# Kernel tuning notes

Hardware: AMD Instinct MI355X
Metric: run time of the kernel (lower is better)

## Reference

```python
import jax, jax.numpy as jnp
import numpy as np

INPUT_DIM, HIDDEN_DIM, OUTPUT_DIM = 64, 256, 64
# AutoNCP(256, 64): inter_and_command=192, command=int(0.4*192)=76, inter=116, motor=64
INTER, COMMAND, MOTOR = 116, 76, 64
SENSORY_FANOUT, INTER_FANOUT, MOTOR_FANIN = 58, 38, 38
B, T = 512, 256


def setup_inputs() -> dict:
    rng = np.random.default_rng(0)
    key = jax.random.key(0)
    d = {}
    # NCP wiring sparsity (binary masks; ncps takes abs() so polarity is irrelevant for the mask)
    m0 = np.zeros((INTER, INPUT_DIM), np.float32)
    for i in range(INPUT_DIM):
        m0[rng.choice(INTER, SENSORY_FANOUT, replace=False), i] = 1.0
    m1 = np.zeros((COMMAND, INTER), np.float32)
    for i in range(INTER):
        m1[rng.choice(COMMAND, INTER_FANOUT, replace=False), i] = 1.0
    m2 = np.zeros((MOTOR, COMMAND), np.float32)
    for o in range(MOTOR):
        m2[o, rng.choice(COMMAND, MOTOR_FANIN, replace=False)] = 1.0
    dims = [(INPUT_DIM, INTER, m0), (INTER, COMMAND, m1), (COMMAND, MOTOR, m2)]
    for l, (fi, h, m) in enumerate(dims):
        cat = fi + h
        # mask shape [h, fi+h]: sparse prev-layer block + all-ones recurrent block (as in WiredCfCCell)
        d[f"mask_{l}"] = jnp.asarray(np.concatenate([m, np.ones((h, h), np.float32)], axis=1))
        bound = float(1.0 / np.sqrt(cat))
        for nm in ("ff1", "ff2", "ta", "tb"):
            key, k1, k2 = jax.random.split(key, 3)
            d[f"w_{nm}_{l}"] = jax.random.uniform(k1, (h, cat), minval=-bound, maxval=bound, dtype=jnp.float32)
            d[f"b_{nm}_{l}"] = jax.random.uniform(k2, (h,), minval=-bound, maxval=bound, dtype=jnp.float32)
    key, k1, k2, kx = jax.random.split(key, 4)
    bound = float(1.0 / np.sqrt(OUTPUT_DIM))
    d["w_fc"] = jax.random.uniform(k1, (OUTPUT_DIM, OUTPUT_DIM), minval=-bound, maxval=bound, dtype=jnp.float32)
    d["b_fc"] = jax.random.uniform(k2, (OUTPUT_DIM,), minval=-bound, maxval=bound, dtype=jnp.float32)
    d["x"] = jax.random.normal(kx, (B, T, INPUT_DIM), dtype=jnp.float32)
    return d


def _cfc_cell(xin, h, w1, b1, w2, b2, wa, ba, wb, bb, mask):
    # CfCCell 'default' mode, no backbone, ts = 1.0
    cat = jnp.concatenate([xin, h], axis=-1)          # [B, fi+h]
    ff1 = jnp.tanh(cat @ (w1 * mask).T + b1)
    ff2 = jnp.tanh(cat @ (w2 * mask).T + b2)
    t_interp = jax.nn.sigmoid(cat @ wa.T + ba + cat @ wb.T + bb)  # sigmoid(t_a*1.0 + t_b)
    return ff1 * (1.0 - t_interp) + t_interp * ff2


def _forward(x, layer_params, masks, w_fc, b_fc):
    bsz = x.shape[0]
    h0 = tuple(jnp.zeros((bsz, h), x.dtype) for h in (INTER, COMMAND, MOTOR))

    def step(hs, xt):
        inp = xt
        new = []
        for l in range(3):  # inter -> command -> motor (structurally distinct layers)
            h = _cfc_cell(inp, hs[l], *layer_params[l], masks[l])
            inp = h
            new.append(h)
        return tuple(new), inp  # motor-layer output per step

    _, ys = jax.lax.scan(step, h0, jnp.swapaxes(x, 0, 1))
    y = jnp.swapaxes(ys, 0, 1)  # [B, T, MOTOR]
    return y @ w_fc.T + b_fc


def reference(x, w_ff1_0, b_ff1_0, w_ff2_0, b_ff2_0, w_ta_0, b_ta_0, w_tb_0, b_tb_0,
              w_ff1_1, b_ff1_1, w_ff2_1, b_ff2_1, w_ta_1, b_ta_1, w_tb_1, b_tb_1,
              w_ff1_2, b_ff1_2, w_ff2_2, b_ff2_2, w_ta_2, b_ta_2, w_tb_2, b_tb_2,
              w_fc, b_fc, mask_0, mask_1, mask_2):
    layer_params = [
        (w_ff1_0, b_ff1_0, w_ff2_0, b_ff2_0, w_ta_0, b_ta_0, w_tb_0, b_tb_0),
        (w_ff1_1, b_ff1_1, w_ff2_1, b_ff2_1, w_ta_1, b_ta_1, w_tb_1, b_tb_1),
        (w_ff1_2, b_ff1_2, w_ff2_2, b_ff2_2, w_ta_2, b_ta_2, w_tb_2, b_tb_2),
    ]
    return _forward(x, layer_params, (mask_0, mask_1, mask_2), w_fc, b_fc)
```

## Files before the change

kernel.cpp:

```cpp
#include <hip/hip_runtime.h>

typedef _Float16 f16x8 __attribute__((ext_vector_type(8)));
typedef _Float16 f16x4 __attribute__((ext_vector_type(4)));
typedef float f32x4 __attribute__((ext_vector_type(4)));

#define NTH 512
#define SEQT 256
#define LD0 200
#define LD1 200
#define LD2 168

struct KArgs { const float* in[30]; float* out; };

__device__ __forceinline__ float fast_tanh(float x) {
  return __fdividef(2.0f, 1.0f + __expf(-2.0f * x)) - 1.0f;
}
__device__ __forceinline__ float fast_sig(float x) {
  return __fdividef(1.0f, 1.0f + __expf(-x));
}

__device__ __forceinline__ f32x4 mfma16(f16x8 a, f16x8 b, f32x4 c) {
  return __builtin_amdgcn_mfma_f32_16x16x32_f16(a, b, c, 0, 0, 0);
}

__device__ __forceinline__ f16x4 combine3(const f32x4 acc[3]) {
  f16x4 v;
  #pragma unroll
  for (int q = 0; q < 4; ++q) {
    const float ff1 = fast_tanh(acc[0][q]);
    const float ff2 = fast_tanh(acc[1][q]);
    const float ti  = fast_sig(acc[2][q]);
    v[q] = (_Float16)(ff1 + ti * (ff2 - ff1));
  }
  return v;
}

template<int BASE, int KT>
__device__ __forceinline__ void load_tile(f16x8* wW, const float* W1, const float* W2,
                                          const float* Wa, const float* Wb,
                                          const float* Mk, int n, int CAT, int H, int kb) {
  #pragma unroll
  for (int kt = 0; kt < KT; ++kt) {
    #pragma unroll
    for (int m = 0; m < 3; ++m) {
      f16x8 f;
      #pragma unroll
      for (int j = 0; j < 8; ++j) {
        const int k = kt * 32 + kb + j;
        float v = 0.f;
        if (n < H && k < CAT) {
          if (m == 0)      v = W1[n*CAT+k] * Mk[n*CAT+k];
          else if (m == 1) v = W2[n*CAT+k] * Mk[n*CAT+k];
          else             v = Wa[n*CAT+k] + Wb[n*CAT+k];
        }
        f[j] = (_Float16)v;
      }
      wW[BASE + m*KT + kt] = f;
    }
  }
}

template<int KT>
__device__ __forceinline__ void loadB(f16x8* B, const _Float16* c, int LD, int r, int kb) {
  #pragma unroll
  for (int kt = 0; kt < KT; ++kt)
    B[kt] = *reinterpret_cast<const f16x8*>(c + r*LD + kt*32 + kb);
}

template<int BASE, int KT>
__device__ __forceinline__ void mma_tile(f32x4 acc[3], const f16x8* wW, const f16x8* B) {
  #pragma unroll
  for (int kt = 0; kt < KT; ++kt)
    #pragma unroll
    for (int m = 0; m < 3; ++m)
      acc[m] = mfma16(wW[BASE + m*KT + kt], B[kt], acc[m]);
}

__device__ __forceinline__ void init3(f32x4 acc[3], const float* sb, int bs, int n0) {
  #pragma unroll
  for (int m = 0; m < 3; ++m)
    acc[m] = *reinterpret_cast<const f32x4*>(sb + m*bs + n0);
}

__device__ __forceinline__ f16x8 loadB8u(const _Float16* p) {
  const f16x4 a = *reinterpret_cast<const f16x4*>(p);
  const f16x4 b = *reinterpret_cast<const f16x4*>(p + 4);
  f16x8 v;
  v[0]=a[0]; v[1]=a[1]; v[2]=a[2]; v[3]=a[3];
  v[4]=b[0]; v[5]=b[1]; v[6]=b[2]; v[7]=b[3];
  return v;
}

__global__ __launch_bounds__(NTH, 2) void ncp_fused(KArgs args) {
  __shared__ __align__(16) _Float16 c0[2][16 * LD0];
  __shared__ __align__(16) _Float16 c1[2][16 * LD1];
  __shared__ __align__(16) _Float16 c2[2][16 * LD2];
  __shared__ __align__(16) _Float16 wt3[15 * 64 * 8];
  __shared__ float b0s[3 * 128], b1s[3 * 80], b2s[3 * 64];

  const int tid  = threadIdx.x;
  const int w    = tid >> 6;
  const int lane = tid & 63;
  const int r    = lane & 15;
  const int g    = lane >> 4;
  const int kb   = g * 8;
  const int wgBase = blockIdx.x * 16;
  const float* __restrict__ xg = args.in[29];
  float* __restrict__ out = args.out;

  f16x8 wW[36], wfc[2];
  f32x4 bfc = {0.f, 0.f, 0.f, 0.f};
  if (w < 4) {
    load_tile<0, 6>(wW, args.in[1], args.in[3], args.in[5], args.in[7], args.in[0],
                    (2*w)*16 + r, 180, 116, kb);
    load_tile<18, 6>(wW, args.in[1], args.in[3], args.in[5], args.in[7], args.in[0],
                     (2*w+1)*16 + r, 180, 116, kb);
    #pragma unroll
    for (int kt = 0; kt < 2; ++kt) {
      f16x8 f;
      #pragma unroll
      for (int j = 0; j < 8; ++j)
        f[j] = (_Float16)args.in[27][(w*16 + r)*64 + kt*32 + kb + j];
      wfc[kt] = f;
    }
    #pragma unroll
    for (int q = 0; q < 4; ++q) bfc[q] = args.in[28][w*16 + 4*g + q];
  } else if (w < 6) {
    load_tile<0, 6>(wW, args.in[10], args.in[12], args.in[14], args.in[16], args.in[9],
                    (2*(w-4))*16 + r, 192, 76, kb);
    load_tile<18, 6>(wW, args.in[10], args.in[12], args.in[14], args.in[16], args.in[9],
                     (2*(w-4)+1)*16 + r, 192, 76, kb);
  } else if (w == 6) {
    load_tile<0, 6>(wW, args.in[10], args.in[12], args.in[14], args.in[16], args.in[9],
                    64 + r, 192, 76, kb);
    load_tile<18, 5>(wW, args.in[19], args.in[21], args.in[23], args.in[25], args.in[18],
                     r, 140, 64, kb);
  } else {
    load_tile<0, 5>(wW, args.in[19], args.in[21], args.in[23], args.in[25], args.in[18],
                    16 + r, 140, 64, kb);
    load_tile<15, 5>(wW, args.in[19], args.in[21], args.in[23], args.in[25], args.in[18],
                     32 + r, 140, 64, kb);
  }

  for (int u = tid; u < 15 * 64; u += NTH) {
    const int ln = u & 63;
    const int ff = u >> 6;
    const int kt = ff % 5, m = ff / 5;
    const int n  = 48 + (ln & 15);
    const int kbb = (ln >> 4) * 8;
    f16x8 f;
    #pragma unroll
    for (int j = 0; j < 8; ++j) {
      const int k = kt*32 + kbb + j;
      float v = 0.f;
      if (k < 140) {
        if (m == 0)      v = args.in[19][n*140+k] * args.in[18][n*140+k];
        else if (m == 1) v = args.in[21][n*140+k] * args.in[18][n*140+k];
        else             v = args.in[23][n*140+k] + args.in[25][n*140+k];
      }
      f[j] = (_Float16)v;
    }
    *reinterpret_cast<f16x8*>(wt3 + (size_t)u * 8) = f;
  }
  if (tid < 128) {
    b0s[tid]       = (tid < 116) ? args.in[2][tid] : 0.f;
    b0s[128 + tid] = (tid < 116) ? args.in[4][tid] : 0.f;
    b0s[256 + tid] = (tid < 116) ? args.in[6][tid] + args.in[8][tid] : 0.f;
  }
  if (tid < 80) {
    b1s[tid]      = (tid < 76) ? args.in[11][tid] : 0.f;
    b1s[80 + tid] = (tid < 76) ? args.in[13][tid] : 0.f;
    b1s[160 + tid]= (tid < 76) ? args.in[15][tid] + args.in[17][tid] : 0.f;
  }
  if (tid < 64) {
    b2s[tid]       = args.in[20][tid];
    b2s[64 + tid]  = args.in[22][tid];
    b2s[128 + tid] = args.in[24][tid] + args.in[26][tid];
  }
  for (int i = tid; i < 2 * 16 * LD0; i += NTH) c0[0][i] = (_Float16)0.f;
  for (int i = tid; i < 2 * 16 * LD1; i += NTH) c1[0][i] = (_Float16)0.f;
  for (int i = tid; i < 2 * 16 * LD2; i += NTH) c2[0][i] = (_Float16)0.f;
  __syncthreads();
  {
    const int rr = tid >> 6, cc = tid & 63;
    c0[0][rr * LD0 + cc]       = (_Float16)xg[((size_t)(wgBase + rr) * SEQT + 0) * 64 + cc];
    c0[0][(8 + rr) * LD0 + cc] = (_Float16)xg[((size_t)(wgBase + 8 + rr) * SEQT + 0) * 64 + cc];
  }
  __syncthreads();

  #pragma unroll 1
  for (int p = 0; p < SEQT + 3; ++p) {
    const int cur = p & 1, nxt = cur ^ 1;

    float xr0, xr1;
    {
      const int tn = (p + 1 < SEQT) ? p + 1 : SEQT - 1;
      xr0 = xg[((size_t)(wgBase + (tid >> 6)) * SEQT + tn) * 64 + (tid & 63)];
      xr1 = xg[((size_t)(wgBase + 8 + (tid >> 6)) * SEQT + tn) * 64 + (tid & 63)];
    }

    if (w < 4) {
      if (p >= 3) {
        f32x4 acc = bfc;
        #pragma unroll
        for (int kt = 0; kt < 2; ++kt) {
          const f16x8 b = loadB8u(c2[cur] + r * LD2 + 76 + kt * 32 + kb);
          acc = mfma16(wfc[kt], b, acc);
        }
        *reinterpret_cast<f32x4*>(out + ((size_t)(wgBase + r) * SEQT + (p - 3)) * 64 + w * 16 + 4 * g) = acc;
      }
      if (p < SEQT) {
        f16x8 B[6]; loadB<6>(B, c0[cur], LD0, r, kb);
        f32x4 aA[3], aB[3];
        const int nA = (2 * w) * 16 + 4 * g;
        const int nB = (2 * w + 1) * 16 + 4 * g;
        init3(aA, b0s, 128, nA);
        init3(aB, b0s, 128, nB);
        mma_tile<0, 6>(aA, wW, B);
        mma_tile<18, 6>(aB, wW, B);
        const f16x4 vA = combine3(aA);
        const f16x4 vB = combine3(aB);
        *reinterpret_cast<f16x4*>(c1[nxt] + r * LD1 + nA)      = vA;
        *reinterpret_cast<f16x4*>(c0[nxt] + r * LD0 + 64 + nA) = vA;
        if (nB < 116) {
          *reinterpret_cast<f16x4*>(c1[nxt] + r * LD1 + nB)      = vB;
          *reinterpret_cast<f16x4*>(c0[nxt] + r * LD0 + 64 + nB) = vB;
        }
      }
    } else if (w < 6) {
      if (p >= 1 && p < SEQT + 1) {
        f16x8 B[6]; loadB<6>(B, c1[cur], LD1, r, kb);
        f32x4 aA[3], aB[3];
        const int nA = (2 * (w - 4)) * 16 + 4 * g;
        const int nB = (2 * (w - 4) + 1) * 16 + 4 * g;
        init3(aA, b1s, 80, nA);
        init3(aB, b1s, 80, nB);
        mma_tile<0, 6>(aA, wW, B);
        mma_tile<18, 6>(aB, wW, B);
        const f16x4 vA = combine3(aA);
        const f16x4 vB = combine3(aB);
        *reinterpret_cast<f16x4*>(c1[nxt] + r * LD1 + 116 + nA) = vA;
        *reinterpret_cast<f16x4*>(c2[nxt] + r * LD2 + nA)       = vA;
        *reinterpret_cast<f16x4*>(c1[nxt] + r * LD1 + 116 + nB) = vB;
        *reinterpret_cast<f16x4*>(c2[nxt] + r * LD2 + nB)       = vB;
      }
    } else if (w == 6) {
      if (p >= 1 && p < SEQT + 1) {
        f16x8 B[6]; loadB<6>(B, c1[cur], LD1, r, kb);
        f32x4 a4[3];
        const int n4 = 64 + 4 * g;
        init3(a4, b1s, 80, n4);
        mma_tile<0, 6>(a4, wW, B);
        const f16x4 v4 = combine3(a4);
        if (n4 < 76) {
          *reinterpret_cast<f16x4*>(c1[nxt] + r * LD1 + 116 + n4) = v4;
          *reinterpret_cast<f16x4*>(c2[nxt] + r * LD2 + n4)       = v4;
        }
      }
      if (p >= 2 && p < SEQT + 2) {
        f16x8 B[5]; loadB<5>(B, c2[cur], LD2, r, kb);
        f32x4 a0[3];
        const int nn = 4 * g;
        init3(a0, b2s, 64, nn);
        mma_tile<18, 5>(a0, wW, B);
        const f16x4 v0 = combine3(a0);
        *reinterpret_cast<f16x4*>(c2[nxt] + r * LD2 + 76 + nn) = v0;
      }
    } else {
      if (p >= 2 && p < SEQT + 2) {
        f16x8 B[5]; loadB<5>(B, c2[cur], LD2, r, kb);
        f32x4 a1[3], a2[3], a3[3];
        const int n1 = 16 + 4 * g, n2 = 32 + 4 * g, n3 = 48 + 4 * g;
        init3(a1, b2s, 64, n1);
        init3(a2, b2s, 64, n2);
        init3(a3, b2s, 64, n3);
        mma_tile<0, 5>(a1, wW, B);
        mma_tile<15, 5>(a2, wW, B);
        #pragma unroll
        for (int kt = 0; kt < 5; ++kt) {
          #pragma unroll
          for (int m = 0; m < 3; ++m) {
            const f16x8 a = *reinterpret_cast<const f16x8*>(wt3 + (size_t)((m * 5 + kt) * 64 + lane) * 8);
            a3[m] = mfma16(a, B[kt], a3[m]);
          }
        }
        const f16x4 v1 = combine3(a1);
        const f16x4 v2 = combine3(a2);
        const f16x4 v3 = combine3(a3);
        *reinterpret_cast<f16x4*>(c2[nxt] + r * LD2 + 76 + n1) = v1;
        *reinterpret_cast<f16x4*>(c2[nxt] + r * LD2 + 76 + n2) = v2;
        *reinterpret_cast<f16x4*>(c2[nxt] + r * LD2 + 76 + n3) = v3;
      }
    }

    if (p < SEQT - 1) {
      const int rr = tid >> 6, cc = tid & 63;
      c0[nxt][rr * LD0 + cc]       = (_Float16)xr0;
      c0[nxt][(8 + rr) * LD0 + cc] = (_Float16)xr1;
    }
    __syncthreads();
  }
}

extern "C" void kernel_launch(void* const* d_in, const int* in_sizes, int n_in,
                              void* d_out, int out_size, void* d_ws, size_t ws_size,
                              hipStream_t stream) {
  KArgs args;
  for (int i = 0; i < 30; ++i) args.in[i] = (const float*)d_in[i];
  args.out = (float*)d_out;
  ncp_fused<<<dim3(32), dim3(NTH), 0, stream>>>(args);
}
```

Baseline: 800.5 us.

## Rebalance output FC onto motor-layer waves and vectorize input staging

Moves the final fully connected projection from the four layer-0 waves to the two motor-layer waves, storing its weights in spare register slots and its bias in shared memory. Input prefetch now uses one float2 load per thread with a pointer that advances each step, instead of two scalar loads with recomputed addresses. Accumulators are reused serially per tile, with writes issued as each tile finishes, to lower register pressure, and MFMA sections are wrapped in s_setprio. The aim is to shorten the critical wave in each barrier-synchronized step, at the cost of more work on waves 6 and 7.

```diff
diff --git a/kernel.cpp b/kernel.cpp
--- a/kernel.cpp
+++ b/kernel.cpp
@@ -2,6 +2,7 @@
 
 typedef _Float16 f16x8 __attribute__((ext_vector_type(8)));
 typedef _Float16 f16x4 __attribute__((ext_vector_type(4)));
+typedef _Float16 f16x2 __attribute__((ext_vector_type(2)));
 typedef float f32x4 __attribute__((ext_vector_type(4)));
 
 #define NTH 512
@@ -96,7 +97,7 @@
   __shared__ __align__(16) _Float16 c1[2][16 * LD1];
   __shared__ __align__(16) _Float16 c2[2][16 * LD2];
   __shared__ __align__(16) _Float16 wt3[15 * 64 * 8];
-  __shared__ float b0s[3 * 128], b1s[3 * 80], b2s[3 * 64];
+  __shared__ float b0s[3 * 128], b1s[3 * 80], b2s[3 * 64], bfcs[64];
 
   const int tid  = threadIdx.x;
   const int w    = tid >> 6;
@@ -106,25 +107,13 @@
   const int kb   = g * 8;
   const int wgBase = blockIdx.x * 16;
   const float* __restrict__ xg = args.in[29];
-  float* __restrict__ out = args.out;
-
-  f16x8 wW[36], wfc[2];
-  f32x4 bfc = {0.f, 0.f, 0.f, 0.f};
+
+  f16x8 wW[37];
   if (w < 4) {
     load_tile<0, 6>(wW, args.in[1], args.in[3], args.in[5], args.in[7], args.in[0],
                     (2*w)*16 + r, 180, 116, kb);
     load_tile<18, 6>(wW, args.in[1], args.in[3], args.in[5], args.in[7], args.in[0],
                      (2*w+1)*16 + r, 180, 116, kb);
-    #pragma unroll
-    for (int kt = 0; kt < 2; ++kt) {
-      f16x8 f;
-      #pragma unroll
-      for (int j = 0; j < 8; ++j)
-        f[j] = (_Float16)args.in[27][(w*16 + r)*64 + kt*32 + kb + j];
-      wfc[kt] = f;
-    }
-    #pragma unroll
-    for (int q = 0; q < 4; ++q) bfc[q] = args.in[28][w*16 + 4*g + q];
   } else if (w < 6) {
     load_tile<0, 6>(wW, args.in[10], args.in[12], args.in[14], args.in[16], args.in[9],
                     (2*(w-4))*16 + r, 192, 76, kb);
@@ -141,6 +130,19 @@
     load_tile<15, 5>(wW, args.in[19], args.in[21], args.in[23], args.in[25], args.in[18],
                      32 + r, 140, 64, kb);
   }
+  if (w >= 6) {
+    const int ot0 = (w - 6) * 2;
+    #pragma unroll
+    for (int tl = 0; tl < 2; ++tl)
+      #pragma unroll
+      for (int kt = 0; kt < 2; ++kt) {
+        f16x8 f;
+        #pragma unroll
+        for (int j = 0; j < 8; ++j)
+          f[j] = (_Float16)args.in[27][((ot0 + tl)*16 + r)*64 + kt*32 + kb + j];
+        wW[33 + tl*2 + kt] = f;
+      }
+  }
 
   for (int u = tid; u < 15 * 64; u += NTH) {
     const int ln = u & 63;
@@ -168,135 +170,172 @@
     b0s[256 + tid] = (tid < 116) ? args.in[6][tid] + args.in[8][tid] : 0.f;
   }
   if (tid < 80) {
-    b1s[tid]      = (tid < 76) ? args.in[11][tid] : 0.f;
-    b1s[80 + tid] = (tid < 76) ? args.in[13][tid] : 0.f;
-    b1s[160 + tid]= (tid < 76) ? args.in[15][tid] + args.in[17][tid] : 0.f;
+    b1s[tid]       = (tid < 76) ? args.in[11][tid] : 0.f;
+    b1s[80 + tid]  = (tid < 76) ? args.in[13][tid] : 0.f;
+    b1s[160 + tid] = (tid < 76) ? args.in[15][tid] + args.in[17][tid] : 0.f;
   }
   if (tid < 64) {
     b2s[tid]       = args.in[20][tid];
     b2s[64 + tid]  = args.in[22][tid];
     b2s[128 + tid] = args.in[24][tid] + args.in[26][tid];
+    bfcs[tid]      = args.in[28][tid];
   }
   for (int i = tid; i < 2 * 16 * LD0; i += NTH) c0[0][i] = (_Float16)0.f;
   for (int i = tid; i < 2 * 16 * LD1; i += NTH) c1[0][i] = (_Float16)0.f;
   for (int i = tid; i < 2 * 16 * LD2; i += NTH) c2[0][i] = (_Float16)0.f;
   __syncthreads();
+  const int rr = tid >> 5, cc = (tid & 31) * 2;
   {
-    const int rr = tid >> 6, cc = tid & 63;
-    c0[0][rr * LD0 + cc]       = (_Float16)xg[((size_t)(wgBase + rr) * SEQT + 0) * 64 + cc];
-    c0[0][(8 + rr) * LD0 + cc] = (_Float16)xg[((size_t)(wgBase + 8 + rr) * SEQT + 0) * 64 + cc];
+    const float2 v = *reinterpret_cast<const float2*>(
+        xg + ((size_t)(wgBase + rr) * SEQT) * 64 + cc);
+    f16x2 pk; pk[0] = (_Float16)v.x; pk[1] = (_Float16)v.y;
+    *reinterpret_cast<f16x2*>(c0[0] + rr * LD0 + cc) = pk;
   }
   __syncthreads();
+
+  const float* xp = xg + ((size_t)(wgBase + rr) * SEQT + 1) * 64 + cc;
+  float* outp = args.out + ((size_t)(wgBase + r) * SEQT) * 64 + (w - 6) * 32 + 4 * g;
 
   #pragma unroll 1
   for (int p = 0; p < SEQT + 3; ++p) {
     const int cur = p & 1, nxt = cur ^ 1;
 
-    float xr0, xr1;
-    {
-      const int tn = (p + 1 < SEQT) ? p + 1 : SEQT - 1;
-      xr0 = xg[((size_t)(wgBase + (tid >> 6)) * SEQT + tn) * 64 + (tid & 63)];
-      xr1 = xg[((size_t)(wgBase + 8 + (tid >> 6)) * SEQT + tn) * 64 + (tid & 63)];
-    }
+    float2 xv;
+    const bool doX = (p < SEQT - 1);
+    if (doX) xv = *reinterpret_cast<const float2*>(xp);
 
     if (w < 4) {
-      if (p >= 3) {
-        f32x4 acc = bfc;
-        #pragma unroll
-        for (int kt = 0; kt < 2; ++kt) {
-          const f16x8 b = loadB8u(c2[cur] + r * LD2 + 76 + kt * 32 + kb);
-          acc = mfma16(wfc[kt], b, acc);
-        }
-        *reinterpret_cast<f32x4*>(out + ((size_t)(wgBase + r) * SEQT + (p - 3)) * 64 + w * 16 + 4 * g) = acc;
-      }
       if (p < SEQT) {
         f16x8 B[6]; loadB<6>(B, c0[cur], LD0, r, kb);
-        f32x4 aA[3], aB[3];
-        const int nA = (2 * w) * 16 + 4 * g;
-        const int nB = (2 * w + 1) * 16 + 4 * g;
-        init3(aA, b0s, 128, nA);
-        init3(aB, b0s, 128, nB);
-        mma_tile<0, 6>(aA, wW, B);
-        mma_tile<18, 6>(aB, wW, B);
-        const f16x4 vA = combine3(aA);
-        const f16x4 vB = combine3(aB);
-        *reinterpret_cast<f16x4*>(c1[nxt] + r * LD1 + nA)      = vA;
-        *reinterpret_cast<f16x4*>(c0[nxt] + r * LD0 + 64 + nA) = vA;
+        f32x4 a[3];
+        const int nA = (2*w)*16 + 4*g;
+        init3(a, b0s, 128, nA);
+        __builtin_amdgcn_s_setprio(1);
+        mma_tile<0, 6>(a, wW, B);
+        __builtin_amdgcn_s_setprio(0);
+        const f16x4 vA = combine3(a);
+        *reinterpret_cast<f16x4*>(c1[nxt] + r*LD1 + nA)      = vA;
+        *reinterpret_cast<f16x4*>(c0[nxt] + r*LD0 + 64 + nA) = vA;
+        const int nB = nA + 16;
+        init3(a, b0s, 128, nB);
+        __builtin_amdgcn_s_setprio(1);
+        mma_tile<18, 6>(a, wW, B);
+        __builtin_amdgcn_s_setprio(0);
+        const f16x4 vB = combine3(a);
         if (nB < 116) {
-          *reinterpret_cast<f16x4*>(c1[nxt] + r * LD1 + nB)      = vB;
-          *reinterpret_cast<f16x4*>(c0[nxt] + r * LD0 + 64 + nB) = vB;
+          *reinterpret_cast<f16x4*>(c1[nxt] + r*LD1 + nB)      = vB;
+          *reinterpret_cast<f16x4*>(c0[nxt] + r*LD0 + 64 + nB) = vB;
         }
       }
     } else if (w < 6) {
-      if (p >= 1 && p < SEQT + 1) {
+      if (p >= 1 && p <= SEQT) {
         f16x8 B[6]; loadB<6>(B, c1[cur], LD1, r, kb);
-        f32x4 aA[3], aB[3];
-        const int nA = (2 * (w - 4)) * 16 + 4 * g;
-        const int nB = (2 * (w - 4) + 1) * 16 + 4 * g;
-        init3(aA, b1s, 80, nA);
-        init3(aB, b1s, 80, nB);
-        mma_tile<0, 6>(aA, wW, B);
-        mma_tile<18, 6>(aB, wW, B);
-        const f16x4 vA = combine3(aA);
-        const f16x4 vB = combine3(aB);
-        *reinterpret_cast<f16x4*>(c1[nxt] + r * LD1 + 116 + nA) = vA;
-        *reinterpret_cast<f16x4*>(c2[nxt] + r * LD2 + nA)       = vA;
-        *reinterpret_cast<f16x4*>(c1[nxt] + r * LD1 + 116 + nB) = vB;
-        *reinterpret_cast<f16x4*>(c2[nxt] + r * LD2 + nB)       = vB;
+        f32x4 a[3];
+        const int nA = (2*(w-4))*16 + 4*g;
+        init3(a, b1s, 80, nA);
+        __builtin_amdgcn_s_setprio(1);
+        mma_tile<0, 6>(a, wW, B);
+        __builtin_amdgcn_s_setprio(0);
+        const f16x4 vA = combine3(a);
+        *reinterpret_cast<f16x4*>(c1[nxt] + r*LD1 + 116 + nA) = vA;
+        *reinterpret_cast<f16x4*>(c2[nxt] + r*LD2 + nA)       = vA;
+        const int nB = nA + 16;
+        init3(a, b1s, 80, nB);
+        __builtin_amdgcn_s_setprio(1);
+        mma_tile<18, 6>(a, wW, B);
+        __builtin_amdgcn_s_setprio(0);
+        const f16x4 vB = combine3(a);
+        *reinterpret_cast<f16x4*>(c1[nxt] + r*LD1 + 116 + nB) = vB;
+        *reinterpret_cast<f16x4*>(c2[nxt] + r*LD2 + nB)       = vB;
       }
     } else if (w == 6) {
-      if (p >= 1 && p < SEQT + 1) {
+      if (p >= 3) {
+        f32x4 fa0 = *reinterpret_cast<const f32x4*>(bfcs + 4*g);
+        f32x4 fa1 = *reinterpret_cast<const f32x4*>(bfcs + 16 + 4*g);
+        const f16x8 hb0 = loadB8u(c2[cur] + r*LD2 + 76 + kb);
+        const f16x8 hb1 = loadB8u(c2[cur] + r*LD2 + 76 + 32 + kb);
+        fa0 = mfma16(wW[33], hb0, fa0); fa0 = mfma16(wW[34], hb1, fa0);
+        fa1 = mfma16(wW[35], hb0, fa1); fa1 = mfma16(wW[36], hb1, fa1);
+        *reinterpret_cast<f32x4*>(outp)      = fa0;
+        *reinterpret_cast<f32x4*>(outp + 16) = fa1;
+        outp += 64;
+      }
+      if (p >= 1 && p <= SEQT) {
         f16x8 B[6]; loadB<6>(B, c1[cur], LD1, r, kb);
-        f32x4 a4[3];
-        const int n4 = 64 + 4 * g;
-        init3(a4, b1s, 80, n4);
-        mma_tile<0, 6>(a4, wW, B);
-        const f16x4 v4 = combine3(a4);
+        f32x4 a[3];
+        const int n4 = 64 + 4*g;
+        init3(a, b1s, 80, n4);
+        __builtin_amdgcn_s_setprio(1);
+        mma_tile<0, 6>(a, wW, B);
+        __builtin_amdgcn_s_setprio(0);
+        const f16x4 v4 = combine3(a);
         if (n4 < 76) {
-          *reinterpret_cast<f16x4*>(c1[nxt] + r * LD1 + 116 + n4) = v4;
-          *reinterpret_cast<f16x4*>(c2[nxt] + r * LD2 + n4)       = v4;
+          *reinterpret_cast<f16x4*>(c1[nxt] + r*LD1 + 116 + n4) = v4;
+          *reinterpret_cast<f16x4*>(c2[nxt] + r*LD2 + n4)       = v4;
         }
       }
-      if (p >= 2 && p < SEQT + 2) {
+      if (p >= 2 && p <= SEQT + 1) {
         f16x8 B[5]; loadB<5>(B, c2[cur], LD2, r, kb);
-        f32x4 a0[3];
-        const int nn = 4 * g;
-        init3(a0, b2s, 64, nn);
-        mma_tile<18, 5>(a0, wW, B);
-        const f16x4 v0 = combine3(a0);
-        *reinterpret_cast<f16x4*>(c2[nxt] + r * LD2 + 76 + nn) = v0;
+        f32x4 a[3];
+        const int nn = 4*g;
+        init3(a, b2s, 64, nn);
+        __builtin_amdgcn_s_setprio(1);
+        mma_tile<18, 5>(a, wW, B);
+        __builtin_amdgcn_s_setprio(0);
+        const f16x4 v0 = combine3(a);
+        *reinterpret_cast<f16x4*>(c2[nxt] + r*LD2 + 76 + nn) = v0;
       }
     } else {
-      if (p >= 2 && p < SEQT + 2) {
+      if (p >= 3) {
+        f32x4 fa0 = *reinterpret_cast<const f32x4*>(bfcs + 32 + 4*g);
+        f32x4 fa1 = *reinterpret_cast<const f32x4*>(bfcs + 48 + 4*g);
+        const f16x8 hb0 = loadB8u(c2[cur] + r*LD2 + 76 + kb);
+        const f16x8 hb1 = loadB8u(c2[cur] + r*LD2 + 76 + 32 + kb);
+        fa0 = mfma16(wW[33], hb0, fa0); fa0 = mfma16(wW[34], hb1, fa0);
+        fa1 = mfma16(wW[35], hb0, fa1); fa1 = mfma16(wW[36], hb1, fa1);
+        *reinterpret_cast<f32x4*>(outp)      = fa0;
+        *reinterpret_cast<f32x4*>(outp + 16) = fa1;
+        outp += 64;
+      }
+      if (p >= 2 && p <= SEQT + 1) {
         f16x8 B[5]; loadB<5>(B, c2[cur], LD2, r, kb);
-        f32x4 a1[3], a2[3], a3[3];
-        const int n1 = 16 + 4 * g, n2 = 32 + 4 * g, n3 = 48 + 4 * g;
-        init3(a1, b2s, 64, n1);
-        init3(a2, b2s, 64, n2);
-        init3(a3, b2s, 64, n3);
-        mma_tile<0, 5>(a1, wW, B);
-        mma_tile<15, 5>(a2, wW, B);
+        f32x4 a[3];
+        const int n1 = 16 + 4*g;
+        init3(a, b2s, 64, n1);
+        __builtin_amdgcn_s_setprio(1);
+        mma_tile<0, 5>(a, wW, B);
+        __builtin_amdgcn_s_setprio(0);
+        const f16x4 v1 = combine3(a);
+        *reinterpret_cast<f16x4*>(c2[nxt] + r*LD2 + 76 + n1) = v1;
+        const int n2 = 32 + 4*g;
+        init3(a, b2s, 64, n2);
+        __builtin_amdgcn_s_setprio(1);
+        mma_tile<15, 5>(a, wW, B);
+        __builtin_amdgcn_s_setprio(0);
+        const f16x4 v2 = combine3(a);
+        *reinterpret_cast<f16x4*>(c2[nxt] + r*LD2 + 76 + n2) = v2;
+        const int n3 = 48 + 4*g;
+        init3(a, b2s, 64, n3);
+        __builtin_amdgcn_s_setprio(1);
         #pragma unroll
         for (int kt = 0; kt < 5; ++kt) {
           #pragma unroll
           for (int m = 0; m < 3; ++m) {
-            const f16x8 a = *reinterpret_cast<const f16x8*>(wt3 + (size_t)((m * 5 + kt) * 64 + lane) * 8);
-            a3[m] = mfma16(a, B[kt], a3[m]);
+            const f16x8 af = *reinterpret_cast<const f16x8*>(
+                wt3 + (size_t)((m*5 + kt)*64 + lane) * 8);
+            a[m] = mfma16(af, B[kt], a[m]);
           }
         }
-        const f16x4 v1 = combine3(a1);
-        const f16x4 v2 = combine3(a2);
-        const f16x4 v3 = combine3(a3);
-        *reinterpret_cast<f16x4*>(c2[nxt] + r * LD2 + 76 + n1) = v1;
-        *reinterpret_cast<f16x4*>(c2[nxt] + r * LD2 + 76 + n2) = v2;
-        *reinterpret_cast<f16x4*>(c2[nxt] + r * LD2 + 76 + n3) = v3;
+        __builtin_amdgcn_s_setprio(0);
+        const f16x4 v3 = combine3(a);
+        *reinterpret_cast<f16x4*>(c2[nxt] + r*LD2 + 76 + n3) = v3;
       }
     }
 
-    if (p < SEQT - 1) {
-      const int rr = tid >> 6, cc = tid & 63;
-      c0[nxt][rr * LD0 + cc]       = (_Float16)xr0;
-      c0[nxt][(8 + rr) * LD0 + cc] = (_Float16)xr1;
+    if (doX) {
+      f16x2 pk; pk[0] = (_Float16)xv.x; pk[1] = (_Float16)xv.y;
+      *reinterpret_cast<f16x2*>(c0[nxt] + rr * LD0 + cc) = pk;
+      xp += 64;
     }
     __syncthreads();
   }
```

Result: no change. 810.9 us (+1.3%).
